# Performance work log

Measured on AMD Instinct MI355X. Metric: run time of the kernel, lower is better.

## Reference

```python
import jax, jax.numpy as jnp
import numpy as np

NUM_HEADS = 12
MASK_BIAS = -1000.0


def setup_inputs() -> dict:
    key = jax.random.key(0)
    k1, k2, k3, k4 = jax.random.split(key, 4)
    B, N, C = 2, 2048, 768
    x = jax.random.normal(k1, (B, N, C), dtype=jnp.float32)
    # key-padding mask: 1.0 = masked-out position (gets -1000 bias), 0.0 = visible
    mask = jax.random.randint(k2, (B, N), 0, 2).astype(jnp.float32)
    qkv_w = jax.random.normal(k3, (3 * C, C), dtype=jnp.float32) * (1.0 / np.sqrt(C))
    proj_w = jax.random.normal(k4, (C, C), dtype=jnp.float32) * (1.0 / np.sqrt(C))
    proj_b = jnp.zeros((C,), dtype=jnp.float32)
    return {"x": x, "mask": mask, "qkv_w": qkv_w, "proj_w": proj_w, "proj_b": proj_b}


def reference(x, mask, qkv_w, proj_w, proj_b):
    B, N, C = x.shape
    H = NUM_HEADS
    D = C // H
    scale = D ** (-0.5)
    # qkv: Linear without bias -> [B, N, 3C] -> [3, B, H, N, D]
    qkv = (x @ qkv_w.T).reshape(B, N, 3, H, D).transpose(2, 0, 3, 1, 4)
    q, k, v = qkv[0], qkv[1], qkv[2]
    # scores [B, H, N, N]
    attn = jnp.einsum("bhqd,bhkd->bhqk", q, k) * scale
    attn = attn + mask[:, None, None, :] * MASK_BIAS
    attn = jax.nn.softmax(attn, axis=-1)
    out = jnp.einsum("bhqk,bhkd->bhqd", attn, v)  # [B, H, N, D]
    out = out.transpose(0, 2, 1, 3).reshape(B, N, C)
    return out @ proj_w.T + proj_b
```

## Files before the change

### kernel.cpp

```cpp
#include <hip/hip_runtime.h>

typedef __bf16 bf16_t;
typedef __bf16 bf16x8 __attribute__((ext_vector_type(8)));
typedef float f32x4 __attribute__((ext_vector_type(4)));

#define NUM_B 2
#define NUM_H 12
#define SEQ_N 2048
#define DIM_C 768
#define HEAD_D 64
#define BH_CNT (NUM_B * NUM_H)
#define MTOK (NUM_B * SEQ_N)
#define SOFTMAX_M 16.0f

#define AS1(p) ((const __attribute__((address_space(1))) void*)(p))
#define AS3(p) ((__attribute__((address_space(3))) void*)(p))

__global__ __launch_bounds__(256) void cvt_kernel(
    const float* __restrict__ s0, const float* __restrict__ s1,
    const float* __restrict__ s2, bf16_t* __restrict__ d0,
    bf16_t* __restrict__ d1, bf16_t* __restrict__ d2, int nb0, int nb1) {
  const int blk = blockIdx.x;
  const float* src;
  bf16_t* dst;
  size_t off;
  if (blk < nb0) {
    src = s0; dst = d0; off = (size_t)blk * 2048;
  } else if (blk < nb0 + nb1) {
    src = s1; dst = d1; off = (size_t)(blk - nb0) * 2048;
  } else {
    src = s2; dst = d2; off = (size_t)(blk - nb0 - nb1) * 2048;
  }
  const size_t i = off + (size_t)threadIdx.x * 8;
  float4 f0 = *reinterpret_cast<const float4*>(&src[i]);
  float4 f1 = *reinterpret_cast<const float4*>(&src[i + 4]);
  union { ushort4 u; bf16_t h[4]; } p0, p1;
  p0.h[0] = (bf16_t)f0.x; p0.h[1] = (bf16_t)f0.y;
  p0.h[2] = (bf16_t)f0.z; p0.h[3] = (bf16_t)f0.w;
  p1.h[0] = (bf16_t)f1.x; p1.h[1] = (bf16_t)f1.y;
  p1.h[2] = (bf16_t)f1.z; p1.h[3] = (bf16_t)f1.w;
  *reinterpret_cast<ushort4*>(&dst[i]) = p0.u;
  *reinterpret_cast<ushort4*>(&dst[i + 4]) = p1.u;
}

template <int EPI>
__global__ __launch_bounds__(256, 3) void gemm_bt_kernel(
    const bf16_t* __restrict__ A, const bf16_t* __restrict__ W,
    const float* __restrict__ bias, void* __restrict__ outv) {
  __shared__ __align__(16) bf16_t As[2][128 * 32];
  __shared__ __align__(16) bf16_t Bs[2][128 * 32];

  const int tid = threadIdx.x;
  const int wave = tid >> 6, lane = tid & 63;
  const int quad = lane >> 4, l16 = lane & 15;
  const int m0 = blockIdx.y * 128, n0 = blockIdx.x * 128;
  const int wm = (wave >> 1) * 64, wn = (wave & 1) * 64;

  f32x4 acc[4][4] = {};

  const int srow = tid >> 2;
  const int scol = ((tid & 3) ^ ((tid >> 3) & 3)) * 8;
  const bf16_t* gA0 = A + (size_t)(m0 + srow) * DIM_C + scol;
  const bf16_t* gA1 = A + (size_t)(m0 + srow + 64) * DIM_C + scol;
  const bf16_t* gB0 = W + (size_t)(n0 + srow) * DIM_C + scol;
  const bf16_t* gB1 = W + (size_t)(n0 + srow + 64) * DIM_C + scol;
  const int lb = wave * 512;

  auto issue = [&](int buf, int k0) {
    __builtin_amdgcn_global_load_lds(AS1(gA0 + k0), AS3(&As[buf][lb]), 16, 0, 0);
    __builtin_amdgcn_global_load_lds(AS1(gA1 + k0), AS3(&As[buf][lb + 2048]), 16, 0, 0);
    __builtin_amdgcn_global_load_lds(AS1(gB0 + k0), AS3(&Bs[buf][lb]), 16, 0, 0);
    __builtin_amdgcn_global_load_lds(AS1(gB1 + k0), AS3(&Bs[buf][lb + 2048]), 16, 0, 0);
  };

  issue(0, 0);
  int cur = 0;
  const int sw = (l16 >> 1) & 3;
  for (int step = 0; step < DIM_C / 32; ++step) {
    __syncthreads();
    if (step + 1 < DIM_C / 32) issue(cur ^ 1, (step + 1) * 32);

    bf16x8 aF[4], bF[4];
#pragma unroll
    for (int mi = 0; mi < 4; ++mi)
      aF[mi] = *reinterpret_cast<const bf16x8*>(
          &As[cur][(wm + mi * 16 + l16) * 32 + ((quad ^ sw) * 8)]);
#pragma unroll
    for (int ni = 0; ni < 4; ++ni)
      bF[ni] = *reinterpret_cast<const bf16x8*>(
          &Bs[cur][(wn + ni * 16 + l16) * 32 + ((quad ^ sw) * 8)]);
#pragma unroll
    for (int mi = 0; mi < 4; ++mi)
#pragma unroll
      for (int ni = 0; ni < 4; ++ni)
        acc[mi][ni] = __builtin_amdgcn_mfma_f32_16x16x32_bf16(aF[mi], bF[ni],
                                                              acc[mi][ni], 0, 0, 0);
    cur ^= 1;
  }

#pragma unroll
  for (int mi = 0; mi < 4; ++mi) {
#pragma unroll
    for (int ni = 0; ni < 4; ++ni) {
      const int gmB = m0 + wm + mi * 16 + quad * 4;
      const int gn = n0 + wn + ni * 16 + l16;
      if (EPI == 0) {
        bf16_t* out = (bf16_t*)outv;
        const int which = gn / DIM_C;
        const int rem = gn - which * DIM_C;
        const int h = rem >> 6, d = rem & 63;
        if (which < 2) {
          const size_t base = (size_t)which * ((size_t)BH_CNT * SEQ_N * HEAD_D);
#pragma unroll
          for (int r = 0; r < 4; ++r) {
            const int gm = gmB + r;
            const int b = gm >> 11, tok = gm & 2047;
            out[base + (((size_t)(b * NUM_H + h) * SEQ_N + tok) * HEAD_D + d)] =
                (bf16_t)acc[mi][ni][r];
          }
        } else {
          const size_t base = 2ull * BH_CNT * SEQ_N * HEAD_D;
          const int b = gmB >> 11, tok0 = gmB & 2047;
          union { ushort4 u; bf16_t h4[4]; } pk;
#pragma unroll
          for (int r = 0; r < 4; ++r) pk.h4[r] = (bf16_t)acc[mi][ni][r];
          *reinterpret_cast<ushort4*>(
              &out[base + (((size_t)(b * NUM_H + h) * HEAD_D + d) * SEQ_N + tok0)]) =
              pk.u;
        }
      } else {
        float* out = (float*)outv;
        const float bv = bias[gn];
#pragma unroll
        for (int r = 0; r < 4; ++r) {
          const int gm = gmB + r;
          out[(size_t)gm * DIM_C + gn] = acc[mi][ni][r] + bv;
        }
      }
    }
  }
}

__global__ __launch_bounds__(256, 3) void attn_kernel(
    const bf16_t* __restrict__ q, const bf16_t* __restrict__ k,
    const bf16_t* __restrict__ vt, const float* __restrict__ mask,
    bf16_t* __restrict__ ctx) {
  __shared__ float biasS[SEQ_N];
  __shared__ __align__(16) bf16_t Ks[2][64 * 64];
  __shared__ __align__(16) bf16_t Vs[2][64 * 64];
  __shared__ __align__(16) bf16_t Ps[4][16][72];

  const int tid = threadIdx.x;
  const int wave = tid >> 6, lane = tid & 63;
  const int quad = lane >> 4, l16 = lane & 15;
  const int bh = blockIdx.y;
  const int b = bh / NUM_H, h = bh - b * NUM_H;
  const int q0 = blockIdx.x * 64 + wave * 16;

  const bf16_t* qb = q + (size_t)bh * SEQ_N * HEAD_D;
  const bf16_t* kb = k + (size_t)bh * SEQ_N * HEAD_D;
  const bf16_t* vtb = vt + (size_t)bh * HEAD_D * SEQ_N;
  const float* mb = mask + (size_t)b * SEQ_N;

  for (int i = tid; i < SEQ_N / 4; i += 256) {
    float4 mv = reinterpret_cast<const float4*>(mb)[i];
    float4 bv = {fmaf(mv.x, -1000.0f, -SOFTMAX_M),
                 fmaf(mv.y, -1000.0f, -SOFTMAX_M),
                 fmaf(mv.z, -1000.0f, -SOFTMAX_M),
                 fmaf(mv.w, -1000.0f, -SOFTMAX_M)};
    reinterpret_cast<float4*>(biasS)[i] = bv;
  }

  bf16x8 qf[2];
#pragma unroll
  for (int ks = 0; ks < 2; ++ks)
    qf[ks] = *reinterpret_cast<const bf16x8*>(
        &qb[(size_t)(q0 + l16) * HEAD_D + ks * 32 + quad * 8]);

  f32x4 acc[4] = {};
  float l_run = 0.0f;

  const int srow = tid >> 3;
  const int scol = ((tid & 7) ^ ((tid >> 3) & 7)) * 8;
  const bf16_t* gK0 = kb + (size_t)srow * HEAD_D + scol;
  const bf16_t* gK1 = kb + (size_t)(srow + 32) * HEAD_D + scol;
  const bf16_t* gV0 = vtb + (size_t)srow * SEQ_N + scol;
  const bf16_t* gV1 = vtb + (size_t)(srow + 32) * SEQ_N + scol;
  const int lb = wave * 512;

  auto issueKV = [&](int buf, int key0) {
    __builtin_amdgcn_global_load_lds(AS1(gK0 + (size_t)key0 * HEAD_D),
                                     AS3(&Ks[buf][lb]), 16, 0, 0);
    __builtin_amdgcn_global_load_lds(AS1(gK1 + (size_t)key0 * HEAD_D),
                                     AS3(&Ks[buf][lb + 2048]), 16, 0, 0);
    __builtin_amdgcn_global_load_lds(AS1(gV0 + key0), AS3(&Vs[buf][lb]), 16, 0, 0);
    __builtin_amdgcn_global_load_lds(AS1(gV1 + key0), AS3(&Vs[buf][lb + 2048]),
                                     16, 0, 0);
  };

  issueKV(0, 0);
  int cur = 0;
  const int swz = l16 & 7;
  for (int key0 = 0; key0 < SEQ_N; key0 += 64) {
    __syncthreads();
    if (key0 + 64 < SEQ_N) issueKV(cur ^ 1, key0 + 64);

    f32x4 s[4];
#pragma unroll
    for (int kt = 0; kt < 4; ++kt) {
      const int row = kt * 16 + l16;
      bf16x8 kf0 = *reinterpret_cast<const bf16x8*>(
          &Ks[cur][row * 64 + ((quad ^ swz) * 8)]);
      bf16x8 kf1 = *reinterpret_cast<const bf16x8*>(
          &Ks[cur][row * 64 + (((4 + quad) ^ swz) * 8)]);
      f32x4 z = {0.0f, 0.0f, 0.0f, 0.0f};
      z = __builtin_amdgcn_mfma_f32_16x16x32_bf16(kf0, qf[0], z, 0, 0, 0);
      s[kt] = __builtin_amdgcn_mfma_f32_16x16x32_bf16(kf1, qf[1], z, 0, 0, 0);
    }

#pragma unroll
    for (int kt = 0; kt < 4; ++kt) {
      float4 bv = *reinterpret_cast<const float4*>(
          &biasS[key0 + kt * 16 + quad * 4]);
      s[kt][0] = __expf(fmaf(s[kt][0], 0.125f, bv.x));
      s[kt][1] = __expf(fmaf(s[kt][1], 0.125f, bv.y));
      s[kt][2] = __expf(fmaf(s[kt][2], 0.125f, bv.z));
      s[kt][3] = __expf(fmaf(s[kt][3], 0.125f, bv.w));
      l_run += s[kt][0] + s[kt][1] + s[kt][2] + s[kt][3];
      union { ushort4 u; bf16_t h4[4]; } pk;
#pragma unroll
      for (int r = 0; r < 4; ++r) pk.h4[r] = (bf16_t)s[kt][r];
      *reinterpret_cast<ushort4*>(&Ps[wave][l16][kt * 16 + quad * 4]) = pk.u;
    }

    bf16x8 pf0 = *reinterpret_cast<const bf16x8*>(&Ps[wave][l16][quad * 8]);
    bf16x8 pf1 = *reinterpret_cast<const bf16x8*>(&Ps[wave][l16][32 + quad * 8]);
#pragma unroll
    for (int dt = 0; dt < 4; ++dt) {
      const int row = dt * 16 + l16;
      bf16x8 vf0 = *reinterpret_cast<const bf16x8*>(
          &Vs[cur][row * 64 + ((quad ^ swz) * 8)]);
      bf16x8 vf1 = *reinterpret_cast<const bf16x8*>(
          &Vs[cur][row * 64 + (((4 + quad) ^ swz) * 8)]);
      acc[dt] = __builtin_amdgcn_mfma_f32_16x16x32_bf16(pf0, vf0, acc[dt], 0, 0, 0);
      acc[dt] = __builtin_amdgcn_mfma_f32_16x16x32_bf16(pf1, vf1, acc[dt], 0, 0, 0);
    }
    cur ^= 1;
  }

  l_run += __shfl_xor(l_run, 16);
  l_run += __shfl_xor(l_run, 32);
  float lr[4];
#pragma unroll
  for (int r = 0; r < 4; ++r) lr[r] = __shfl(l_run, quad * 4 + r, 16);
#pragma unroll
  for (int dt = 0; dt < 4; ++dt)
#pragma unroll
    for (int r = 0; r < 4; ++r) {
      const int tok = q0 + quad * 4 + r;
      ctx[((size_t)b * SEQ_N + tok) * DIM_C + h * HEAD_D + dt * 16 + l16] =
          (bf16_t)(acc[dt][r] / lr[r]);
    }
}

extern "C" void kernel_launch(void* const* d_in, const int* in_sizes, int n_in,
                              void* d_out, int out_size, void* d_ws,
                              size_t ws_size, hipStream_t stream) {
  const float* x = (const float*)d_in[0];
  const float* mask = (const float*)d_in[1];
  const float* qkv_w = (const float*)d_in[2];
  const float* proj_w = (const float*)d_in[3];
  const float* proj_b = (const float*)d_in[4];
  float* out = (float*)d_out;

  const size_t nx = (size_t)MTOK * DIM_C;
  const size_t nqw = (size_t)3 * DIM_C * DIM_C;
  const size_t npw = (size_t)DIM_C * DIM_C;
  const size_t per = (size_t)BH_CNT * SEQ_N * HEAD_D;

  bf16_t* xb = (bf16_t*)d_ws;
  bf16_t* qwb = xb + nx;
  bf16_t* pwb = qwb + nqw;
  bf16_t* qkv = pwb + npw;
  bf16_t* ctx = qkv + 3 * per;

  const int nb0 = (int)(nx / 2048), nb1 = (int)(nqw / 2048),
            nb2 = (int)(npw / 2048);

  cvt_kernel<<<nb0 + nb1 + nb2, 256, 0, stream>>>(x, qkv_w, proj_w, xb, qwb, pwb,
                                                  nb0, nb1);
  gemm_bt_kernel<0><<<dim3(3 * DIM_C / 128, MTOK / 128), 256, 0, stream>>>(
      xb, qwb, nullptr, qkv);
  attn_kernel<<<dim3(SEQ_N / 64, BH_CNT), 256, 0, stream>>>(
      qkv, qkv + per, qkv + 2 * per, mask, ctx);
  gemm_bt_kernel<1><<<dim3(DIM_C / 128, MTOK / 128), 256, 0, stream>>>(
      ctx, pwb, proj_b, out);
}
```

Baseline: 164.6 us.

## Fold key mask into V and compute softmax denominators with MFMA

The key-padding mask is no longer applied as a bias in the attention loop. Instead V is multiplied by (1-mask) in the QKV GEMM epilogue, and the softmax row sums come from an extra MFMA of P against a bf16 (1-mask) vector. Q is pre-scaled by log2(e)/sqrt(D) so the inner loop needs only exp2 with no fma or bias load, and the fixed max-offset is dropped. The P scratch buffer is XOR-swizzled to cut LDS bank conflicts. The GEMMs use 64-row M tiles with occupancy 4 for more blocks. Without any max subtraction, large scores risk overflow or reduced precision.

After: 171.2 us. 1.04x slower.

```diff
diff --git a/kernel.cpp b/kernel.cpp
--- a/kernel.cpp
+++ b/kernel.cpp
@@ -11,29 +11,38 @@
 #define HEAD_D 64
 #define BH_CNT (NUM_B * NUM_H)
 #define MTOK (NUM_B * SEQ_N)
-#define SOFTMAX_M 16.0f
+#define QSCALE 0.1803368801111137f
 
 #define AS1(p) ((const __attribute__((address_space(1))) void*)(p))
 #define AS3(p) ((__attribute__((address_space(3))) void*)(p))
 
 __global__ __launch_bounds__(256) void cvt_kernel(
     const float* __restrict__ s0, const float* __restrict__ s1,
-    const float* __restrict__ s2, bf16_t* __restrict__ d0,
-    bf16_t* __restrict__ d1, bf16_t* __restrict__ d2, int nb0, int nb1) {
+    const float* __restrict__ s2, const float* __restrict__ msk,
+    bf16_t* __restrict__ d0, bf16_t* __restrict__ d1, bf16_t* __restrict__ d2,
+    bf16_t* __restrict__ dw, int nb0, int nb1, int nb2) {
   const int blk = blockIdx.x;
   const float* src;
   bf16_t* dst;
   size_t off;
+  bool isw = false;
   if (blk < nb0) {
     src = s0; dst = d0; off = (size_t)blk * 2048;
   } else if (blk < nb0 + nb1) {
     src = s1; dst = d1; off = (size_t)(blk - nb0) * 2048;
+  } else if (blk < nb0 + nb1 + nb2) {
+    src = s2; dst = d2; off = (size_t)(blk - nb0 - nb1) * 2048;
   } else {
-    src = s2; dst = d2; off = (size_t)(blk - nb0 - nb1) * 2048;
+    src = msk; dst = dw; off = (size_t)(blk - nb0 - nb1 - nb2) * 2048;
+    isw = true;
   }
   const size_t i = off + (size_t)threadIdx.x * 8;
   float4 f0 = *reinterpret_cast<const float4*>(&src[i]);
   float4 f1 = *reinterpret_cast<const float4*>(&src[i + 4]);
+  if (isw) {
+    f0 = {1.0f - f0.x, 1.0f - f0.y, 1.0f - f0.z, 1.0f - f0.w};
+    f1 = {1.0f - f1.x, 1.0f - f1.y, 1.0f - f1.z, 1.0f - f1.w};
+  }
   union { ushort4 u; bf16_t h[4]; } p0, p1;
   p0.h[0] = (bf16_t)f0.x; p0.h[1] = (bf16_t)f0.y;
   p0.h[2] = (bf16_t)f0.z; p0.h[3] = (bf16_t)f0.w;
@@ -44,31 +53,30 @@
 }
 
 template <int EPI>
-__global__ __launch_bounds__(256, 3) void gemm_bt_kernel(
+__global__ __launch_bounds__(256, 4) void gemm_bt_kernel(
     const bf16_t* __restrict__ A, const bf16_t* __restrict__ W,
-    const float* __restrict__ bias, void* __restrict__ outv) {
-  __shared__ __align__(16) bf16_t As[2][128 * 32];
+    const float* __restrict__ bias, const float* __restrict__ mask,
+    void* __restrict__ outv) {
+  __shared__ __align__(16) bf16_t As[2][64 * 32];
   __shared__ __align__(16) bf16_t Bs[2][128 * 32];
 
   const int tid = threadIdx.x;
   const int wave = tid >> 6, lane = tid & 63;
   const int quad = lane >> 4, l16 = lane & 15;
-  const int m0 = blockIdx.y * 128, n0 = blockIdx.x * 128;
-  const int wm = (wave >> 1) * 64, wn = (wave & 1) * 64;
-
-  f32x4 acc[4][4] = {};
+  const int m0 = blockIdx.y * 64, n0 = blockIdx.x * 128;
+  const int wm = (wave >> 1) * 32, wn = (wave & 1) * 64;
+
+  f32x4 acc[2][4] = {};
 
   const int srow = tid >> 2;
   const int scol = ((tid & 3) ^ ((tid >> 3) & 3)) * 8;
-  const bf16_t* gA0 = A + (size_t)(m0 + srow) * DIM_C + scol;
-  const bf16_t* gA1 = A + (size_t)(m0 + srow + 64) * DIM_C + scol;
+  const bf16_t* gA = A + (size_t)(m0 + srow) * DIM_C + scol;
   const bf16_t* gB0 = W + (size_t)(n0 + srow) * DIM_C + scol;
   const bf16_t* gB1 = W + (size_t)(n0 + srow + 64) * DIM_C + scol;
   const int lb = wave * 512;
 
   auto issue = [&](int buf, int k0) {
-    __builtin_amdgcn_global_load_lds(AS1(gA0 + k0), AS3(&As[buf][lb]), 16, 0, 0);
-    __builtin_amdgcn_global_load_lds(AS1(gA1 + k0), AS3(&As[buf][lb + 2048]), 16, 0, 0);
+    __builtin_amdgcn_global_load_lds(AS1(gA + k0), AS3(&As[buf][lb]), 16, 0, 0);
     __builtin_amdgcn_global_load_lds(AS1(gB0 + k0), AS3(&Bs[buf][lb]), 16, 0, 0);
     __builtin_amdgcn_global_load_lds(AS1(gB1 + k0), AS3(&Bs[buf][lb + 2048]), 16, 0, 0);
   };
@@ -80,9 +88,9 @@
     __syncthreads();
     if (step + 1 < DIM_C / 32) issue(cur ^ 1, (step + 1) * 32);
 
-    bf16x8 aF[4], bF[4];
-#pragma unroll
-    for (int mi = 0; mi < 4; ++mi)
+    bf16x8 aF[2], bF[4];
+#pragma unroll
+    for (int mi = 0; mi < 2; ++mi)
       aF[mi] = *reinterpret_cast<const bf16x8*>(
           &As[cur][(wm + mi * 16 + l16) * 32 + ((quad ^ sw) * 8)]);
 #pragma unroll
@@ -90,7 +98,7 @@
       bF[ni] = *reinterpret_cast<const bf16x8*>(
           &Bs[cur][(wn + ni * 16 + l16) * 32 + ((quad ^ sw) * 8)]);
 #pragma unroll
-    for (int mi = 0; mi < 4; ++mi)
+    for (int mi = 0; mi < 2; ++mi)
 #pragma unroll
       for (int ni = 0; ni < 4; ++ni)
         acc[mi][ni] = __builtin_amdgcn_mfma_f32_16x16x32_bf16(aF[mi], bF[ni],
@@ -99,7 +107,7 @@
   }
 
 #pragma unroll
-  for (int mi = 0; mi < 4; ++mi) {
+  for (int mi = 0; mi < 2; ++mi) {
 #pragma unroll
     for (int ni = 0; ni < 4; ++ni) {
       const int gmB = m0 + wm + mi * 16 + quad * 4;
@@ -109,21 +117,23 @@
         const int which = gn / DIM_C;
         const int rem = gn - which * DIM_C;
         const int h = rem >> 6, d = rem & 63;
+        const int b = gmB >> 11, tok0 = gmB & 2047;
         if (which < 2) {
+          const float sc = (which == 0) ? QSCALE : 1.0f;
           const size_t base = (size_t)which * ((size_t)BH_CNT * SEQ_N * HEAD_D);
 #pragma unroll
           for (int r = 0; r < 4; ++r) {
-            const int gm = gmB + r;
-            const int b = gm >> 11, tok = gm & 2047;
-            out[base + (((size_t)(b * NUM_H + h) * SEQ_N + tok) * HEAD_D + d)] =
-                (bf16_t)acc[mi][ni][r];
+            out[base + (((size_t)(b * NUM_H + h) * SEQ_N + tok0 + r) * HEAD_D + d)] =
+                (bf16_t)(acc[mi][ni][r] * sc);
           }
         } else {
           const size_t base = 2ull * BH_CNT * SEQ_N * HEAD_D;
-          const int b = gmB >> 11, tok0 = gmB & 2047;
+          float4 mv = *reinterpret_cast<const float4*>(&mask[b * SEQ_N + tok0]);
           union { ushort4 u; bf16_t h4[4]; } pk;
-#pragma unroll
-          for (int r = 0; r < 4; ++r) pk.h4[r] = (bf16_t)acc[mi][ni][r];
+          pk.h4[0] = (bf16_t)(acc[mi][ni][0] * (1.0f - mv.x));
+          pk.h4[1] = (bf16_t)(acc[mi][ni][1] * (1.0f - mv.y));
+          pk.h4[2] = (bf16_t)(acc[mi][ni][2] * (1.0f - mv.z));
+          pk.h4[3] = (bf16_t)(acc[mi][ni][3] * (1.0f - mv.w));
           *reinterpret_cast<ushort4*>(
               &out[base + (((size_t)(b * NUM_H + h) * HEAD_D + d) * SEQ_N + tok0)]) =
               pk.u;
@@ -141,14 +151,13 @@
   }
 }
 
-__global__ __launch_bounds__(256, 3) void attn_kernel(
+__global__ __launch_bounds__(256, 4) void attn_kernel(
     const bf16_t* __restrict__ q, const bf16_t* __restrict__ k,
-    const bf16_t* __restrict__ vt, const float* __restrict__ mask,
+    const bf16_t* __restrict__ vt, const bf16_t* __restrict__ wv,
     bf16_t* __restrict__ ctx) {
-  __shared__ float biasS[SEQ_N];
   __shared__ __align__(16) bf16_t Ks[2][64 * 64];
   __shared__ __align__(16) bf16_t Vs[2][64 * 64];
-  __shared__ __align__(16) bf16_t Ps[4][16][72];
+  __shared__ __align__(16) bf16_t Ps[4][1024];
 
   const int tid = threadIdx.x;
   const int wave = tid >> 6, lane = tid & 63;
@@ -160,16 +169,7 @@
   const bf16_t* qb = q + (size_t)bh * SEQ_N * HEAD_D;
   const bf16_t* kb = k + (size_t)bh * SEQ_N * HEAD_D;
   const bf16_t* vtb = vt + (size_t)bh * HEAD_D * SEQ_N;
-  const float* mb = mask + (size_t)b * SEQ_N;
-
-  for (int i = tid; i < SEQ_N / 4; i += 256) {
-    float4 mv = reinterpret_cast<const float4*>(mb)[i];
-    float4 bv = {fmaf(mv.x, -1000.0f, -SOFTMAX_M),
-                 fmaf(mv.y, -1000.0f, -SOFTMAX_M),
-                 fmaf(mv.z, -1000.0f, -SOFTMAX_M),
-                 fmaf(mv.w, -1000.0f, -SOFTMAX_M)};
-    reinterpret_cast<float4*>(biasS)[i] = bv;
-  }
+  const bf16_t* wb = wv + (size_t)b * SEQ_N;
 
   bf16x8 qf[2];
 #pragma unroll
@@ -178,7 +178,7 @@
         &qb[(size_t)(q0 + l16) * HEAD_D + ks * 32 + quad * 8]);
 
   f32x4 acc[4] = {};
-  float l_run = 0.0f;
+  f32x4 acc_l = {};
 
   const int srow = tid >> 3;
   const int scol = ((tid & 7) ^ ((tid >> 3) & 7)) * 8;
@@ -201,6 +201,7 @@
   issueKV(0, 0);
   int cur = 0;
   const int swz = l16 & 7;
+  const int psbase = wave * 1024 + l16 * 64;
   for (int key0 = 0; key0 < SEQ_N; key0 += 64) {
     __syncthreads();
     if (key0 + 64 < SEQ_N) issueKV(cur ^ 1, key0 + 64);
@@ -220,21 +221,25 @@
 
 #pragma unroll
     for (int kt = 0; kt < 4; ++kt) {
-      float4 bv = *reinterpret_cast<const float4*>(
-          &biasS[key0 + kt * 16 + quad * 4]);
-      s[kt][0] = __expf(fmaf(s[kt][0], 0.125f, bv.x));
-      s[kt][1] = __expf(fmaf(s[kt][1], 0.125f, bv.y));
-      s[kt][2] = __expf(fmaf(s[kt][2], 0.125f, bv.z));
-      s[kt][3] = __expf(fmaf(s[kt][3], 0.125f, bv.w));
-      l_run += s[kt][0] + s[kt][1] + s[kt][2] + s[kt][3];
       union { ushort4 u; bf16_t h4[4]; } pk;
-#pragma unroll
-      for (int r = 0; r < 4; ++r) pk.h4[r] = (bf16_t)s[kt][r];
-      *reinterpret_cast<ushort4*>(&Ps[wave][l16][kt * 16 + quad * 4]) = pk.u;
-    }
-
-    bf16x8 pf0 = *reinterpret_cast<const bf16x8*>(&Ps[wave][l16][quad * 8]);
-    bf16x8 pf1 = *reinterpret_cast<const bf16x8*>(&Ps[wave][l16][32 + quad * 8]);
+      pk.h4[0] = (bf16_t)exp2f(s[kt][0]);
+      pk.h4[1] = (bf16_t)exp2f(s[kt][1]);
+      pk.h4[2] = (bf16_t)exp2f(s[kt][2]);
+      pk.h4[3] = (bf16_t)exp2f(s[kt][3]);
+      const int c = kt * 2 + (quad >> 1);
+      *reinterpret_cast<ushort4*>(
+          &Ps[0][psbase + ((c ^ swz) << 3) + ((quad & 1) << 2)]) = pk.u;
+    }
+
+    bf16x8 pf0 = *reinterpret_cast<const bf16x8*>(
+        &Ps[0][psbase + ((quad ^ swz) << 3)]);
+    bf16x8 pf1 = *reinterpret_cast<const bf16x8*>(
+        &Ps[0][psbase + (((4 + quad) ^ swz) << 3)]);
+    bf16x8 wf0 = *reinterpret_cast<const bf16x8*>(&wb[key0 + quad * 8]);
+    bf16x8 wf1 = *reinterpret_cast<const bf16x8*>(&wb[key0 + 32 + quad * 8]);
+    acc_l = __builtin_amdgcn_mfma_f32_16x16x32_bf16(pf0, wf0, acc_l, 0, 0, 0);
+    acc_l = __builtin_amdgcn_mfma_f32_16x16x32_bf16(pf1, wf1, acc_l, 0, 0, 0);
+
 #pragma unroll
     for (int dt = 0; dt < 4; ++dt) {
       const int row = dt * 16 + l16;
@@ -248,18 +253,16 @@
     cur ^= 1;
   }
 
-  l_run += __shfl_xor(l_run, 16);
-  l_run += __shfl_xor(l_run, 32);
-  float lr[4];
-#pragma unroll
-  for (int r = 0; r < 4; ++r) lr[r] = __shfl(l_run, quad * 4 + r, 16);
+  float rl[4];
+#pragma unroll
+  for (int r = 0; r < 4; ++r) rl[r] = 1.0f / acc_l[r];
 #pragma unroll
   for (int dt = 0; dt < 4; ++dt)
 #pragma unroll
     for (int r = 0; r < 4; ++r) {
       const int tok = q0 + quad * 4 + r;
       ctx[((size_t)b * SEQ_N + tok) * DIM_C + h * HEAD_D + dt * 16 + l16] =
-          (bf16_t)(acc[dt][r] / lr[r]);
+          (bf16_t)(acc[dt][r] * rl[r]);
     }
 }
 
@@ -276,23 +279,25 @@
   const size_t nx = (size_t)MTOK * DIM_C;
   const size_t nqw = (size_t)3 * DIM_C * DIM_C;
   const size_t npw = (size_t)DIM_C * DIM_C;
+  const size_t nmask = (size_t)NUM_B * SEQ_N;
   const size_t per = (size_t)BH_CNT * SEQ_N * HEAD_D;
 
   bf16_t* xb = (bf16_t*)d_ws;
   bf16_t* qwb = xb + nx;
   bf16_t* pwb = qwb + nqw;
-  bf16_t* qkv = pwb + npw;
+  bf16_t* wvb = pwb + npw;
+  bf16_t* qkv = wvb + nmask;
   bf16_t* ctx = qkv + 3 * per;
 
   const int nb0 = (int)(nx / 2048), nb1 = (int)(nqw / 2048),
-            nb2 = (int)(npw / 2048);
-
-  cvt_kernel<<<nb0 + nb1 + nb2, 256, 0, stream>>>(x, qkv_w, proj_w, xb, qwb, pwb,
-                                                  nb0, nb1);
-  gemm_bt_kernel<0><<<dim3(3 * DIM_C / 128, MTOK / 128), 256, 0, stream>>>(
-      xb, qwb, nullptr, qkv);
+            nb2 = (int)(npw / 2048), nbm = (int)(nmask / 2048);
+
+  cvt_kernel<<<nb0 + nb1 + nb2 + nbm, 256, 0, stream>>>(
+      x, qkv_w, proj_w, mask, xb, qwb, pwb, wvb, nb0, nb1, nb2);
+  gemm_bt_kernel<0><<<dim3(3 * DIM_C / 128, MTOK / 64), 256, 0, stream>>>(
+      xb, qwb, nullptr, mask, qkv);
   attn_kernel<<<dim3(SEQ_N / 64, BH_CNT), 256, 0, stream>>>(
-      qkv, qkv + per, qkv + 2 * per, mask, ctx);
-  gemm_bt_kernel<1><<<dim3(DIM_C / 128, MTOK / 128), 256, 0, stream>>>(
-      ctx, pwb, proj_b, out);
+      qkv, qkv + per, qkv + 2 * per, wvb, ctx);
+  gemm_bt_kernel<1><<<dim3(DIM_C / 128, MTOK / 64), 256, 0, stream>>>(
+      ctx, pwb, proj_b, nullptr, out);
 }
```
